# Performance work log

Measured on AMD Instinct MI355X. Metric: run time of the kernel, lower is better.

The kernel has to match this reference:

```python
import jax, jax.numpy as jnp
import numpy as np

WAVE_LEN = 1000.0

def rank_embedding(rank_dim, feat_dim):
    half = feat_dim // 2
    dim_mat = jnp.arange(half, dtype=jnp.float32) / half
    inv = 1.0 / jnp.power(WAVE_LEN, dim_mat)            # [half]
    mul = jnp.arange(rank_dim, dtype=jnp.float32)[:, None] * inv[None, :]  # [K, half]
    return jnp.concatenate([jnp.sin(mul), jnp.cos(mul)], axis=-1)          # [K, feat_dim]

def setup_inputs() -> dict:
    key = jax.random.key(0)
    ks = jax.random.split(key, 16)
    K, NS, NC, D, DF, H, DK = 2048, 18, 19, 1024, 128, 16, 64
    s = 0.02
    return {
        "size_scores": jax.random.normal(ks[0], (1, K, NS), jnp.float32),
        "size_residuals_normalized": jax.random.normal(ks[1], (1, K, NS, 3), jnp.float32),
        "sem_cls_scores": jax.random.normal(ks[2], (K, NC), jnp.float32),
        "appearance_features": jax.random.normal(ks[3], (K, D), jnp.float32),
        "mean_size_arr": jax.random.uniform(ks[4], (NS, 3), jnp.float32, 0.1, 1.0),
        "w_rank": jax.random.normal(ks[5], (D, DF), jnp.float32) * s,
        "b_rank": jnp.zeros((DF,), jnp.float32),
        "w_roi": jax.random.normal(ks[6], (D, DF), jnp.float32) * s,
        "b_roi": jnp.zeros((DF,), jnp.float32),
        "Wq": jax.random.normal(ks[7], (H, DF, DK), jnp.float32) * s,
        "Wk": jax.random.normal(ks[8], (H, DF, DK), jnp.float32) * s,
        "Wv": jax.random.normal(ks[9], (H, D, DK), jnp.float32) * s,
        "w_logit": jax.random.normal(ks[10], (D, 1), jnp.float32) * s,
        "b_logit": jnp.zeros((1,), jnp.float32),
    }

def reference(size_scores, size_residuals_normalized, sem_cls_scores,
              appearance_features, mean_size_arr,
              w_rank, b_rank, w_roi, b_roi, Wq, Wk, Wv, w_logit, b_logit):
    K, D = appearance_features.shape
    # --- predicted box size: gather residual for argmax size class ---
    pred_size_class = jnp.argmax(size_scores, axis=-1)                     # [1,K]
    size_residuals = size_residuals_normalized * mean_size_arr[None, None] # [1,K,NS,3]
    pred_size_residual = jnp.take_along_axis(
        size_residuals, pred_size_class[..., None, None], axis=2)[:, :, 0, :]  # [1,K,3]
    psc = pred_size_class[0]                                               # [K]
    box_size = mean_size_arr[psc] + pred_size_residual[0]                  # [K,3]
    # --- semantic class prob ---
    prob_all = jax.nn.softmax(sem_cls_scores, axis=-1)                     # [K,NC]
    prob = jnp.max(prob_all, axis=-1)                                      # [K]
    prob_argmax = jnp.argmax(prob_all, axis=-1)                            # [K]
    cls_bbox = box_size                                                    # [K,3]
    # --- background masking (jit-friendly analog of nonzero filtering):
    # background (class 0) proposals get key -1 so they sort to the end with score 0.
    fg = prob_argmax > 0
    sort_key = jnp.where(fg, prob, -1.0)
    order = jnp.argsort(-sort_key)                                         # descending
    sorted_prob = jnp.where(fg[order], prob[order], 0.0)                   # [K]
    sorted_labels = prob_argmax[order]                                     # [K]
    sorted_cls_bboxes = cls_bbox[order]                                    # [K,3]
    sorted_features = appearance_features[order]                           # [K,D]
    # --- rank embedding + roi embedding ---
    emb = rank_embedding(K, D)                                             # [K,D]
    nms_rank = emb @ w_rank + b_rank                                       # [K,DF]
    roi = sorted_features @ w_roi + b_roi                                  # [K,DF]
    e = nms_rank + roi                                                     # [K,DF]
    # --- relation-module self-attention: Q/K from embedding, V from features ---
    dk = Wq.shape[-1]
    q = jnp.einsum('kd,hde->hke', e, Wq)                                   # [H,K,dk]
    k = jnp.einsum('kd,hde->hke', e, Wk)
    scores = jnp.einsum('hke,hme->hkm', q, k) / jnp.sqrt(jnp.float32(dk))  # [H,K,K]
    attn = jax.nn.softmax(scores, axis=-1)
    v = jnp.einsum('kf,hfe->hke', sorted_features, Wv)                     # [H,K,dk]
    o = jnp.einsum('hkm,hme->hke', attn, v)                                # [H,K,dk]
    o = jnp.transpose(o, (1, 0, 2)).reshape(K, -1)                         # [K,D]
    attn_out = sorted_features + o                                         # residual
    # --- nms logit ---
    logit = attn_out @ w_logit + b_logit                                   # [K,1]
    s1 = jax.nn.sigmoid(logit).reshape(-1)
    nms_scores = s1 * sorted_prob
    return nms_scores, sorted_labels - 1, sorted_cls_bboxes
```

## Files before the change

kernel.cpp:

```cpp
#include <hip/hip_runtime.h>

#define KP 2048
#define DD 1024
#define DF 128
#define NH 16
#define DKK 64
#define NSS 18
#define NCC 19
#define NCH 4
#define CHUNK 512

typedef __attribute__((ext_vector_type(8))) short short8;
typedef __attribute__((ext_vector_type(4))) short short4_t;
typedef __attribute__((ext_vector_type(4))) float f32x4;

__device__ __forceinline__ short f2bf(float x){
    unsigned u = __float_as_uint(x);
    u += 0x7fffu + ((u >> 16) & 1u);
    return (short)(u >> 16);
}

__device__ __forceinline__ void gl2lds16(const void* g, void* l){
    __builtin_amdgcn_global_load_lds((const __attribute__((address_space(1))) void*)g,
                                     (__attribute__((address_space(3))) void*)l, 16, 0, 0);
}

__global__ void prep_kernel(const float* __restrict__ size_scores,
                            const float* __restrict__ srn,
                            const float* __restrict__ sem,
                            const float* __restrict__ mean,
                            float* __restrict__ box, int* __restrict__ label,
                            double* __restrict__ probd, double* __restrict__ keyd){
    int k = blockIdx.x * blockDim.x + threadIdx.x;
    if (k >= KP) return;
    const float* ss = size_scores + k * NSS;
    int psc = 0; float bs = ss[0];
    for (int s = 1; s < NSS; s++){ float v = ss[s]; if (v > bs){ bs = v; psc = s; } }
    for (int c = 0; c < 3; c++){
        float m = mean[psc * 3 + c];
        float r = srn[k * (NSS * 3) + psc * 3 + c];
        box[k * 3 + c] = m + r * m;
    }
    const float* cs = sem + k * NCC;
    double mx = (double)cs[0]; int lab = 0;
    for (int c = 1; c < NCC; c++){ double v = (double)cs[c]; if (v > mx){ mx = v; lab = c; } }
    double sum = 0.0;
    for (int c = 0; c < NCC; c++) sum += exp((double)cs[c] - mx);
    double prob = 1.0 / sum;
    probd[k] = prob;
    label[k] = lab;
    keyd[k]  = (lab > 0) ? prob : -1.0;
}

__global__ __launch_bounds__(256) void rank_kernel(const double* __restrict__ keyd,
                                                   const int* __restrict__ label,
                                                   const double* __restrict__ probd,
                                                   const float* __restrict__ box,
                                                   int* __restrict__ order, float* __restrict__ sprob,
                                                   float* __restrict__ out){
    int i = blockIdx.x, t = threadIdx.x;
    double ki = keyd[i];
    const double2* k2 = (const double2*)keyd;
    int r = 0;
    #pragma unroll
    for (int p = 0; p < KP / 2 / 256; p++){
        int idx2 = p * 256 + t;
        double2 kj = k2[idx2];
        int j0 = idx2 * 2;
        r += (int)(kj.x > ki) + (int)((kj.x == ki) & (j0 < i));
        r += (int)(kj.y > ki) + (int)((kj.y == ki) & (j0 + 1 < i));
    }
    #pragma unroll
    for (int off = 32; off > 0; off >>= 1) r += __shfl_down(r, off);
    __shared__ int red[4];
    if ((t & 63) == 0) red[t >> 6] = r;
    __syncthreads();
    if (t == 0){
        int rk = red[0] + red[1] + red[2] + red[3];
        order[rk] = i;
        sprob[rk] = (label[i] > 0) ? (float)probd[i] : 0.f;
        out[KP + rk] = (float)(label[i] - 1);
        out[2 * KP + 3 * rk + 0] = box[i * 3 + 0];
        out[2 * KP + 3 * rk + 1] = box[i * 3 + 1];
        out[2 * KP + 3 * rk + 2] = box[i * 3 + 2];
    }
}

__global__ __launch_bounds__(256) void af_kernel(const float* __restrict__ app,
                                                 const int* __restrict__ order,
                                                 short* __restrict__ af){
    int pos = blockIdx.x, t = threadIdx.x;
    int ord = order[pos];
    float4 v = ((const float4*)(app + (size_t)ord * DD))[t];
    short4_t g = { f2bf(v.x), f2bf(v.y), f2bf(v.z), f2bf(v.w) };
    *(short4_t*)(af + (size_t)pos * 2048 + 1024 + t * 4) = g;
    short4_t e;
    #pragma unroll
    for (int i = 0; i < 4; i++){
        int j = t * 4 + i, jj = j & 511;
        float inv = exp2f(-(float)jj * 0.0194644224310197f);
        float arg = (float)pos * inv;
        e[i] = f2bf((j < 512) ? __sinf(arg) : __cosf(arg));
    }
    *(short4_t*)(af + (size_t)pos * 2048 + t * 4) = e;
}

__global__ __launch_bounds__(256) void convw_kernel(const float* __restrict__ w_rank,
                                                    const float* __restrict__ w_roi,
                                                    const float* __restrict__ Wq,
                                                    const float* __restrict__ Wk,
                                                    const float* __restrict__ Wv,
                                                    const float* __restrict__ w_logit,
                                                    short* __restrict__ wcat,
                                                    short* __restrict__ qkT,
                                                    short* __restrict__ uT){
    int b = blockIdx.x;
    if (b >= 128){
        int i = b - 128;
        int h = i >> 2;
        int f = ((i & 3) << 8) + threadIdx.x;
        const float* wv = Wv + (size_t)h * DD * DKK + (size_t)f * DKK;
        const float* wlh = w_logit + h * DKK;
        float s = 0.f;
        #pragma unroll
        for (int e = 0; e < DKK; e++) s += wv[e] * wlh[e];
        uT[h * DD + f] = f2bf(s);
        return;
    }
    __shared__ float tile[64][65];
    const float* src; short* dst; int sstride, dstride, r0, c0, doff;
    float scale = 1.0f;
    if (b < 32){        src = w_rank; dst = wcat; sstride = DF; dstride = 2048;
                        r0 = (b >> 1) * 64; c0 = (b & 1) * 64; doff = 0; }
    else if (b < 64){   int i = b - 32; src = w_roi; dst = wcat; sstride = DF; dstride = 2048;
                        r0 = (i >> 1) * 64; c0 = (i & 1) * 64; doff = 1024; }
    else if (b < 96){   int i = b - 64; int h = i >> 1;
                        src = Wq + (size_t)h * DF * DKK; dst = qkT + (size_t)h * DKK * DF;
                        sstride = DKK; dstride = DF; r0 = (i & 1) * 64; c0 = 0; doff = 0;
                        scale = 0.125f; }
    else {              int i = b - 96; int h = i >> 1;
                        src = Wk + (size_t)h * DF * DKK; dst = qkT + (size_t)(1024 + h * DKK) * DF;
                        sstride = DKK; dstride = DF; r0 = (i & 1) * 64; c0 = 0; doff = 0; }
    int tx = threadIdx.x & 63, ty = threadIdx.x >> 6;
    #pragma unroll
    for (int p = 0; p < 16; p++){
        int r = p * 4 + ty;
        tile[r][tx] = src[(size_t)(r0 + r) * sstride + c0 + tx];
    }
    __syncthreads();
    #pragma unroll
    for (int p = 0; p < 16; p++){
        int r = p * 4 + ty;
        dst[(size_t)(c0 + r) * dstride + doff + r0 + tx] = f2bf(tile[tx][r] * scale);
    }
}

__global__ __launch_bounds__(256) void gemm_lds(const short* __restrict__ A,
                                                const short* __restrict__ BT,
                                                void* __restrict__ C,
                                                int lda, int ldb, int N,
                                                int klen, size_t slabstride, int mode){
    int w = threadIdx.x >> 6, lane = threadIdx.x & 63;
    int quad = lane >> 4, l16 = lane & 15;
    int m0 = blockIdx.x * 64, n0 = blockIdx.y * 64;
    int kb = blockIdx.z * klen;

    __shared__ __align__(16) short alds[64 * 64];
    __shared__ __align__(16) short blds[64 * 64];

    int p0 = w * 64 + lane;
    int r0 = p0 >> 3, q0 = ((p0 & 7) ^ (r0 & 7)) * 8;
    int p1 = p0 + 256;
    int r1 = p1 >> 3, q1 = ((p1 & 7) ^ (r1 & 7)) * 8;
    short* adst0 = alds + w * 512;
    short* adst1 = alds + 2048 + w * 512;
    short* bdst0 = blds + w * 512;
    short* bdst1 = blds + 2048 + w * 512;
    const short* asrc0 = A + (size_t)(m0 + r0) * lda + kb + q0;
    const short* asrc1 = A + (size_t)(m0 + r1) * lda + kb + q1;
    const short* bsrc0 = BT + (size_t)(n0 + r0) * ldb + kb + q0;
    const short* bsrc1 = BT + (size_t)(n0 + r1) * ldb + kb + q1;

    f32x4 acc[4];
    for (int c = 0; c < 4; c++) acc[c] = (f32x4){0.f, 0.f, 0.f, 0.f};

    for (int kt = 0; kt < klen; kt += 64){
        __syncthreads();
        gl2lds16(asrc0 + kt, adst0);
        gl2lds16(asrc1 + kt, adst1);
        gl2lds16(bsrc0 + kt, bdst0);
        gl2lds16(bsrc1 + kt, bdst1);
        __syncthreads();
        int arow = w * 16 + l16;
        #pragma unroll
        for (int s = 0; s < 2; s++){
            short8 a = *(const short8*)(alds + arow * 64 + (((s * 4 + quad) ^ (l16 & 7)) * 8));
            #pragma unroll
            for (int c = 0; c < 4; c++){
                int brow = c * 16 + l16;
                short8 b = *(const short8*)(blds + brow * 64 + (((s * 4 + quad) ^ (l16 & 7)) * 8));
                acc[c] = __builtin_amdgcn_mfma_f32_16x16x32_bf16(a, b, acc[c], 0, 0, 0);
            }
        }
    }
    int mrow = m0 + w * 16 + quad * 4;
    #pragma unroll
    for (int c = 0; c < 4; c++){
        #pragma unroll
        for (int r = 0; r < 4; r++){
            size_t idx = (size_t)(mrow + r) * N + n0 + c * 16 + l16;
            if (mode == 2) ((short*)C)[idx] = f2bf(acc[c][r]);
            else ((float*)C + (size_t)blockIdx.z * slabstride)[idx] = acc[c][r];
        }
    }
}

__global__ __launch_bounds__(256) void combine_e_kernel(const float* __restrict__ es,
                                                        const float* __restrict__ b_rank,
                                                        const float* __restrict__ b_roi,
                                                        short* __restrict__ e_bf){
    int tid = blockIdx.x * 256 + threadIdx.x;
    int base = tid * 4;
    int n = base & (DF - 1);
    float4 s = *(const float4*)(es + base);
    #pragma unroll
    for (int c = 1; c < 4; c++){
        float4 t = *(const float4*)(es + (size_t)c * KP * DF + base);
        s.x += t.x; s.y += t.y; s.z += t.z; s.w += t.w;
    }
    float4 br = *(const float4*)(b_rank + n);
    float4 bo = *(const float4*)(b_roi + n);
    short4_t o = { f2bf(s.x + br.x + bo.x), f2bf(s.y + br.y + bo.y),
                   f2bf(s.z + br.z + bo.z), f2bf(s.w + br.w + bo.w) };
    *(short4_t*)(e_bf + base) = o;
}

__global__ __launch_bounds__(256) void vw_kernel(const short* __restrict__ af,
                                                 const short* __restrict__ uT,
                                                 float* __restrict__ vwT){
    int w = threadIdx.x >> 6, lane = threadIdx.x & 63;
    int quad = lane >> 4, l16 = lane & 15;
    int m0 = blockIdx.x * 64 + w * 16;
    f32x4 acc = (f32x4){0.f, 0.f, 0.f, 0.f};
    const short* arow = af + (size_t)(m0 + l16) * 2048 + 1024 + quad * 8;
    const short* brow = uT + (size_t)l16 * DD + quad * 8;
    for (int k0 = 0; k0 < DD; k0 += 32){
        short8 a = *(const short8*)(arow + k0);
        short8 b = *(const short8*)(brow + k0);
        acc = __builtin_amdgcn_mfma_f32_16x16x32_bf16(a, b, acc, 0, 0, 0);
    }
    #pragma unroll
    for (int r = 0; r < 4; r++)
        vwT[(size_t)l16 * KP + m0 + quad * 4 + r] = acc[r];
}

__global__ __launch_bounds__(256, 4) void attn_kernel(const short* __restrict__ qk,
                                                      const float* __restrict__ vwT,
                                                      float* __restrict__ pl,
                                                      float* __restrict__ pwl){
    int qt = blockIdx.x, h = blockIdx.y, ch = blockIdx.z;
    int tid = threadIdx.x;
    int w = tid >> 6, lane = tid & 63, quad = lane >> 4, l16 = lane & 15;
    int qb = qt * 128;

    __shared__ __align__(16) short klds[64 * 64];

    short8 aq[2][2];
    #pragma unroll
    for (int t = 0; t < 2; t++){
        const short* qrow = qk + (size_t)(qb + t * 64 + w * 16 + l16) * 2048 + h * DKK;
        aq[t][0] = *(const short8*)(qrow + quad * 8);
        aq[t][1] = *(const short8*)(qrow + 32 + quad * 8);
    }

    float lpart[2][4] = {{0.f,0.f,0.f,0.f},{0.f,0.f,0.f,0.f}};
    float wpart[2][4] = {{0.f,0.f,0.f,0.f},{0.f,0.f,0.f,0.f}};

    int seg0 = w * 128 + lane;
    int row0 = seg0 >> 3, c80 = (seg0 & 7) ^ (row0 & 7);
    int seg1 = seg0 + 64;
    int row1 = seg1 >> 3, c81 = (seg1 & 7) ^ (row1 & 7);
    short* kl0 = klds + (size_t)(w * 128) * 8;
    short* kl1 = klds + (size_t)(w * 128 + 64) * 8;

    for (int m0 = ch * CHUNK; m0 < (ch + 1) * CHUNK; m0 += 64){
        __syncthreads();
        gl2lds16(qk + (size_t)(m0 + row0) * 2048 + 1024 + h * DKK + c80 * 8, kl0);
        gl2lds16(qk + (size_t)(m0 + row1) * 2048 + 1024 + h * DKK + c81 * 8, kl1);
        float vwv[4];
        #pragma unroll
        for (int c = 0; c < 4; c++)
            vwv[c] = vwT[(size_t)h * KP + m0 + c * 16 + l16];
        __syncthreads();

        #pragma unroll
        for (int t = 0; t < 2; t++){
            #pragma unroll
            for (int c = 0; c < 4; c++){
                int r = c * 16 + l16, sw = r & 7;
                short8 b0 = *(const short8*)(klds + r * 64 + (quad ^ sw) * 8);
                short8 b1 = *(const short8*)(klds + r * 64 + ((quad + 4) ^ sw) * 8);
                f32x4 acc = (f32x4){0.f, 0.f, 0.f, 0.f};
                acc = __builtin_amdgcn_mfma_f32_16x16x32_bf16(aq[t][0], b0, acc, 0, 0, 0);
                acc = __builtin_amdgcn_mfma_f32_16x16x32_bf16(aq[t][1], b1, acc, 0, 0, 0);
                #pragma unroll
                for (int rr = 0; rr < 4; rr++){
                    float e = __expf(acc[rr]);
                    lpart[t][rr] += e;
                    wpart[t][rr] += e * vwv[c];
                }
            }
        }
    }

    #pragma unroll
    for (int t = 0; t < 2; t++){
        #pragma unroll
        for (int rr = 0; rr < 4; rr++){
            float v = lpart[t][rr], x = wpart[t][rr];
            v += __shfl_xor(v, 1); x += __shfl_xor(x, 1);
            v += __shfl_xor(v, 2); x += __shfl_xor(x, 2);
            v += __shfl_xor(v, 4); x += __shfl_xor(x, 4);
            v += __shfl_xor(v, 8); x += __shfl_xor(x, 8);
            lpart[t][rr] = v; wpart[t][rr] = x;
        }
        if (l16 == 0){
            int qr0 = qb + t * 64 + w * 16;
            #pragma unroll
            for (int rr = 0; rr < 4; rr++){
                size_t idx = ((size_t)ch * NH + h) * KP + qr0 + quad * 4 + rr;
                pl[idx]  = lpart[t][rr];
                pwl[idx] = wpart[t][rr];
            }
        }
    }
}

__global__ __launch_bounds__(256) void final_kernel(const float* __restrict__ app,
                                                    const int* __restrict__ order,
                                                    const float* __restrict__ pl,
                                                    const float* __restrict__ pwl,
                                                    const float* __restrict__ w_logit,
                                                    const float* __restrict__ b_logit,
                                                    const float* __restrict__ sprob,
                                                    float* __restrict__ out){
    int pos = blockIdx.x, t = threadIdx.x;
    int ord = order[pos];
    float4 a = *(const float4*)(app + (size_t)ord * DD + t * 4);
    float4 wv = *(const float4*)(w_logit + t * 4);
    float partial = a.x * wv.x + a.y * wv.y + a.z * wv.z + a.w * wv.w;
    for (int off = 32; off > 0; off >>= 1) partial += __shfl_down(partial, off);
    __shared__ float red[4];
    __shared__ float hsum[NH];
    if ((t & 63) == 0) red[t >> 6] = partial;
    if (t < NH){
        float l = 0.f, x = 0.f;
        #pragma unroll
        for (int c = 0; c < NCH; c++){
            size_t idx = ((size_t)c * NH + t) * KP + pos;
            l += pl[idx]; x += pwl[idx];
        }
        hsum[t] = x / l;
    }
    __syncthreads();
    if (t == 0){
        float logit = red[0] + red[1] + red[2] + red[3] + b_logit[0];
        #pragma unroll
        for (int h = 0; h < NH; h++) logit += hsum[h];
        float s1 = 1.f / (1.f + __expf(-logit));
        out[pos] = s1 * sprob[pos];
    }
}

extern "C" void kernel_launch(void* const* d_in, const int* in_sizes, int n_in,
                              void* d_out, int out_size, void* d_ws, size_t ws_size,
                              hipStream_t stream){
    (void)in_sizes; (void)n_in; (void)out_size; (void)ws_size;
    const float* size_scores = (const float*)d_in[0];
    const float* srn     = (const float*)d_in[1];
    const float* sem     = (const float*)d_in[2];
    const float* app     = (const float*)d_in[3];
    const float* mean    = (const float*)d_in[4];
    const float* w_rank  = (const float*)d_in[5];
    const float* b_rank  = (const float*)d_in[6];
    const float* w_roi   = (const float*)d_in[7];
    const float* b_roi   = (const float*)d_in[8];
    const float* Wq      = (const float*)d_in[9];
    const float* Wk      = (const float*)d_in[10];
    const float* Wv      = (const float*)d_in[11];
    const float* w_logit = (const float*)d_in[12];
    const float* b_logit = (const float*)d_in[13];
    float* out = (float*)d_out;

    char* ws = (char*)d_ws;
    size_t off = 0;
    auto alloc = [&](size_t n) -> char* {
        char* p = ws + off;
        off = (off + n + 255) & ~(size_t)255;
        return p;
    };
    float*  box    = (float*) alloc((size_t)KP * 3 * 4);
    int*    label  = (int*)   alloc((size_t)KP * 4);
    double* probd  = (double*)alloc((size_t)KP * 8);
    double* keyd   = (double*)alloc((size_t)KP * 8);
    int*    order  = (int*)   alloc((size_t)KP * 4);
    float*  sprob  = (float*) alloc((size_t)KP * 4);
    short*  wcat   = (short*) alloc((size_t)DF * 2048 * 2);
    short*  qkT    = (short*) alloc((size_t)2048 * DF * 2);
    short*  uT     = (short*) alloc((size_t)NH * DD * 2);
    short*  e_bf   = (short*) alloc((size_t)KP * DF * 2);
    short*  qk_bf  = (short*) alloc((size_t)KP * 2048 * 2);
    float*  vwT    = (float*) alloc((size_t)NH * KP * 4);
    float*  pl     = (float*) alloc((size_t)NCH * NH * KP * 4);
    float*  pwl    = (float*) alloc((size_t)NCH * NH * KP * 4);
    char*   X      = alloc((size_t)12 * 1024 * 1024);
    short*  af     = (short*)X;
    float*  es     = (float*)(X + (size_t)8 * 1024 * 1024);

    prep_kernel<<<KP / 256, 256, 0, stream>>>(size_scores, srn, sem, mean, box, label, probd, keyd);
    rank_kernel<<<KP, 256, 0, stream>>>(keyd, label, probd, box, order, sprob, out);
    af_kernel<<<KP, 256, 0, stream>>>(app, order, af);
    convw_kernel<<<192, 256, 0, stream>>>(w_rank, w_roi, Wq, Wk, Wv, w_logit, wcat, qkT, uT);
    gemm_lds<<<dim3(KP / 64, DF / 64, 4), 256, 0, stream>>>(af, wcat, es, 2048, 2048, DF, 512,
                                                            (size_t)KP * DF, 0);
    combine_e_kernel<<<(KP * DF / 4) / 256, 256, 0, stream>>>(es, b_rank, b_roi, e_bf);
    gemm_lds<<<dim3(KP / 64, 2048 / 64, 1), 256, 0, stream>>>(e_bf, qkT, qk_bf, DF, DF, 2048, DF,
                                                              0, 2);
    vw_kernel<<<KP / 64, 256, 0, stream>>>(af, uT, vwT);
    attn_kernel<<<dim3(KP / 128, NH, NCH), 256, 0, stream>>>(qk_bf, vwT, pl, pwl);
    final_kernel<<<KP, 256, 0, stream>>>(app, order, pl, pwl, w_logit, b_logit, sprob, out);
}
```

Before: 150.5 us.

## Fuse pipeline stages into fewer launches and finalize logits via atomic counter

Merges prep with weight conversion, rank with the feature scatter and logit dot product, the e-combine with the vw GEMV, and attention with the final sigmoid. The last block per query tile, found through an agent-scope atomic counter, does the final reduction. The first GEMM's split-K goes from 4 to 16 and the attention key chunks from 4 to 2. This removes several kernel launches and their global round trips, and gives the first GEMM more parallelism. The cost is a larger split-K partial buffer, more reduction reads, and atomics plus fences at the end of attention.

```diff
diff --git a/kernel.cpp b/kernel.cpp
--- a/kernel.cpp
+++ b/kernel.cpp
@@ -7,8 +7,9 @@
 #define DKK 64
 #define NSS 18
 #define NCC 19
-#define NCH 4
-#define CHUNK 512
+#define NCH 2
+#define CHUNK 1024
+#define SPLK 16
 
 typedef __attribute__((ext_vector_type(8))) short short8;
 typedef __attribute__((ext_vector_type(4))) short short4_t;
@@ -25,100 +26,41 @@
                                      (__attribute__((address_space(3))) void*)l, 16, 0, 0);
 }
 
-__global__ void prep_kernel(const float* __restrict__ size_scores,
-                            const float* __restrict__ srn,
-                            const float* __restrict__ sem,
-                            const float* __restrict__ mean,
-                            float* __restrict__ box, int* __restrict__ label,
-                            double* __restrict__ probd, double* __restrict__ keyd){
-    int k = blockIdx.x * blockDim.x + threadIdx.x;
-    if (k >= KP) return;
-    const float* ss = size_scores + k * NSS;
-    int psc = 0; float bs = ss[0];
-    for (int s = 1; s < NSS; s++){ float v = ss[s]; if (v > bs){ bs = v; psc = s; } }
-    for (int c = 0; c < 3; c++){
-        float m = mean[psc * 3 + c];
-        float r = srn[k * (NSS * 3) + psc * 3 + c];
-        box[k * 3 + c] = m + r * m;
-    }
-    const float* cs = sem + k * NCC;
-    double mx = (double)cs[0]; int lab = 0;
-    for (int c = 1; c < NCC; c++){ double v = (double)cs[c]; if (v > mx){ mx = v; lab = c; } }
-    double sum = 0.0;
-    for (int c = 0; c < NCC; c++) sum += exp((double)cs[c] - mx);
-    double prob = 1.0 / sum;
-    probd[k] = prob;
-    label[k] = lab;
-    keyd[k]  = (lab > 0) ? prob : -1.0;
-}
-
-__global__ __launch_bounds__(256) void rank_kernel(const double* __restrict__ keyd,
-                                                   const int* __restrict__ label,
-                                                   const double* __restrict__ probd,
-                                                   const float* __restrict__ box,
-                                                   int* __restrict__ order, float* __restrict__ sprob,
-                                                   float* __restrict__ out){
-    int i = blockIdx.x, t = threadIdx.x;
-    double ki = keyd[i];
-    const double2* k2 = (const double2*)keyd;
-    int r = 0;
-    #pragma unroll
-    for (int p = 0; p < KP / 2 / 256; p++){
-        int idx2 = p * 256 + t;
-        double2 kj = k2[idx2];
-        int j0 = idx2 * 2;
-        r += (int)(kj.x > ki) + (int)((kj.x == ki) & (j0 < i));
-        r += (int)(kj.y > ki) + (int)((kj.y == ki) & (j0 + 1 < i));
-    }
-    #pragma unroll
-    for (int off = 32; off > 0; off >>= 1) r += __shfl_down(r, off);
-    __shared__ int red[4];
-    if ((t & 63) == 0) red[t >> 6] = r;
-    __syncthreads();
-    if (t == 0){
-        int rk = red[0] + red[1] + red[2] + red[3];
-        order[rk] = i;
-        sprob[rk] = (label[i] > 0) ? (float)probd[i] : 0.f;
-        out[KP + rk] = (float)(label[i] - 1);
-        out[2 * KP + 3 * rk + 0] = box[i * 3 + 0];
-        out[2 * KP + 3 * rk + 1] = box[i * 3 + 1];
-        out[2 * KP + 3 * rk + 2] = box[i * 3 + 2];
-    }
-}
-
-__global__ __launch_bounds__(256) void af_kernel(const float* __restrict__ app,
-                                                 const int* __restrict__ order,
-                                                 short* __restrict__ af){
-    int pos = blockIdx.x, t = threadIdx.x;
-    int ord = order[pos];
-    float4 v = ((const float4*)(app + (size_t)ord * DD))[t];
-    short4_t g = { f2bf(v.x), f2bf(v.y), f2bf(v.z), f2bf(v.w) };
-    *(short4_t*)(af + (size_t)pos * 2048 + 1024 + t * 4) = g;
-    short4_t e;
-    #pragma unroll
-    for (int i = 0; i < 4; i++){
-        int j = t * 4 + i, jj = j & 511;
-        float inv = exp2f(-(float)jj * 0.0194644224310197f);
-        float arg = (float)pos * inv;
-        e[i] = f2bf((j < 512) ? __sinf(arg) : __cosf(arg));
-    }
-    *(short4_t*)(af + (size_t)pos * 2048 + t * 4) = e;
-}
-
-__global__ __launch_bounds__(256) void convw_kernel(const float* __restrict__ w_rank,
-                                                    const float* __restrict__ w_roi,
-                                                    const float* __restrict__ Wq,
-                                                    const float* __restrict__ Wk,
-                                                    const float* __restrict__ Wv,
-                                                    const float* __restrict__ w_logit,
-                                                    short* __restrict__ wcat,
-                                                    short* __restrict__ qkT,
-                                                    short* __restrict__ uT){
-    int b = blockIdx.x;
+__global__ __launch_bounds__(256) void prep_convw_kernel(const float* __restrict__ size_scores,
+        const float* __restrict__ srn, const float* __restrict__ sem,
+        const float* __restrict__ mean,
+        const float* __restrict__ w_rank, const float* __restrict__ w_roi,
+        const float* __restrict__ Wq, const float* __restrict__ Wk,
+        const float* __restrict__ Wv, const float* __restrict__ w_logit,
+        float* __restrict__ box, int* __restrict__ label,
+        double* __restrict__ probd, double* __restrict__ keyd,
+        short* __restrict__ wcat, short* __restrict__ qkT, short* __restrict__ uT){
+    int bid = blockIdx.x, t = threadIdx.x;
+    if (bid < 8){
+        int k = bid * 256 + t;
+        const float* ss = size_scores + k * NSS;
+        int psc = 0; float bs = ss[0];
+        for (int s = 1; s < NSS; s++){ float v = ss[s]; if (v > bs){ bs = v; psc = s; } }
+        for (int c = 0; c < 3; c++){
+            float m = mean[psc * 3 + c];
+            float r = srn[k * (NSS * 3) + psc * 3 + c];
+            box[k * 3 + c] = m + r * m;
+        }
+        const float* cs = sem + k * NCC;
+        double mx = (double)cs[0]; int lab = 0;
+        for (int c = 1; c < NCC; c++){ double v = (double)cs[c]; if (v > mx){ mx = v; lab = c; } }
+        double sum = 0.0;
+        for (int c = 0; c < NCC; c++) sum += exp((double)cs[c] - mx);
+        probd[k] = 1.0 / sum;
+        label[k] = lab;
+        keyd[k]  = (lab > 0) ? (1.0 / sum) : -1.0;
+        return;
+    }
+    int b = bid - 8;
     if (b >= 128){
         int i = b - 128;
         int h = i >> 2;
-        int f = ((i & 3) << 8) + threadIdx.x;
+        int f = ((i & 3) << 8) + t;
         const float* wv = Wv + (size_t)h * DD * DKK + (size_t)f * DKK;
         const float* wlh = w_logit + h * DKK;
         float s = 0.f;
@@ -141,18 +83,77 @@
     else {              int i = b - 96; int h = i >> 1;
                         src = Wk + (size_t)h * DF * DKK; dst = qkT + (size_t)(1024 + h * DKK) * DF;
                         sstride = DKK; dstride = DF; r0 = (i & 1) * 64; c0 = 0; doff = 0; }
-    int tx = threadIdx.x & 63, ty = threadIdx.x >> 6;
-    #pragma unroll
-    for (int p = 0; p < 16; p++){
-        int r = p * 4 + ty;
+    int tx = t & 63, ty = t >> 6;
+    #pragma unroll
+    for (int pp = 0; pp < 16; pp++){
+        int r = pp * 4 + ty;
         tile[r][tx] = src[(size_t)(r0 + r) * sstride + c0 + tx];
     }
     __syncthreads();
     #pragma unroll
-    for (int p = 0; p < 16; p++){
-        int r = p * 4 + ty;
+    for (int pp = 0; pp < 16; pp++){
+        int r = pp * 4 + ty;
         dst[(size_t)(c0 + r) * dstride + doff + r0 + tx] = f2bf(tile[tx][r] * scale);
     }
+}
+
+__global__ __launch_bounds__(256) void rank_af_kernel(const double* __restrict__ keyd,
+        const int* __restrict__ label, const double* __restrict__ probd,
+        const float* __restrict__ box, const float* __restrict__ app,
+        const float* __restrict__ w_logit,
+        int* __restrict__ order, float* __restrict__ sprob, float* __restrict__ dotl,
+        short* __restrict__ af, unsigned* __restrict__ cnt, float* __restrict__ out){
+    int i = blockIdx.x, t = threadIdx.x;
+    if (i < 16 && t == 0) cnt[i] = 0;
+    __shared__ int redi[4];
+    __shared__ float redf[4];
+    __shared__ int rks;
+    double ki = keyd[i];
+    const double2* k2 = (const double2*)keyd;
+    int r = 0;
+    #pragma unroll
+    for (int pp = 0; pp < KP / 2 / 256; pp++){
+        int idx2 = pp * 256 + t;
+        double2 kj = k2[idx2];
+        int j0 = idx2 * 2;
+        r += (int)(kj.x > ki) + (int)((kj.x == ki) & (j0 < i));
+        r += (int)(kj.y > ki) + (int)((kj.y == ki) & (j0 + 1 < i));
+    }
+    #pragma unroll
+    for (int off = 32; off > 0; off >>= 1) r += __shfl_down(r, off);
+    if ((t & 63) == 0) redi[t >> 6] = r;
+    __syncthreads();
+    if (t == 0){
+        int rk = redi[0] + redi[1] + redi[2] + redi[3];
+        rks = rk;
+        order[rk] = i;
+        sprob[rk] = (label[i] > 0) ? (float)probd[i] : 0.f;
+        out[KP + rk] = (float)(label[i] - 1);
+        out[2 * KP + 3 * rk + 0] = box[i * 3 + 0];
+        out[2 * KP + 3 * rk + 1] = box[i * 3 + 1];
+        out[2 * KP + 3 * rk + 2] = box[i * 3 + 2];
+    }
+    __syncthreads();
+    int pos = rks;
+    float4 v = ((const float4*)(app + (size_t)i * DD))[t];
+    float4 wv = ((const float4*)w_logit)[t];
+    short4_t gg = { f2bf(v.x), f2bf(v.y), f2bf(v.z), f2bf(v.w) };
+    *(short4_t*)(af + (size_t)pos * 2048 + 1024 + t * 4) = gg;
+    float partial = v.x * wv.x + v.y * wv.y + v.z * wv.z + v.w * wv.w;
+    #pragma unroll
+    for (int off = 32; off > 0; off >>= 1) partial += __shfl_down(partial, off);
+    if ((t & 63) == 0) redf[t >> 6] = partial;
+    short4_t e;
+    #pragma unroll
+    for (int ii = 0; ii < 4; ii++){
+        int j = t * 4 + ii, jj = j & 511;
+        float inv = exp2f(-(float)jj * 0.0194644224310197f);
+        float arg = (float)pos * inv;
+        e[ii] = f2bf((j < 512) ? __sinf(arg) : __cosf(arg));
+    }
+    *(short4_t*)(af + (size_t)pos * 2048 + t * 4) = e;
+    __syncthreads();
+    if (t == 0) dotl[pos] = redf[0] + redf[1] + redf[2] + redf[3];
 }
 
 __global__ __launch_bounds__(256) void gemm_lds(const short* __restrict__ A,
@@ -215,64 +216,63 @@
     }
 }
 
-__global__ __launch_bounds__(256) void combine_e_kernel(const float* __restrict__ es,
-                                                        const float* __restrict__ b_rank,
-                                                        const float* __restrict__ b_roi,
-                                                        short* __restrict__ e_bf){
-    int tid = blockIdx.x * 256 + threadIdx.x;
-    int base = tid * 4;
-    int n = base & (DF - 1);
-    float4 s = *(const float4*)(es + base);
-    #pragma unroll
-    for (int c = 1; c < 4; c++){
-        float4 t = *(const float4*)(es + (size_t)c * KP * DF + base);
-        s.x += t.x; s.y += t.y; s.z += t.z; s.w += t.w;
-    }
-    float4 br = *(const float4*)(b_rank + n);
-    float4 bo = *(const float4*)(b_roi + n);
-    short4_t o = { f2bf(s.x + br.x + bo.x), f2bf(s.y + br.y + bo.y),
-                   f2bf(s.z + br.z + bo.z), f2bf(s.w + br.w + bo.w) };
-    *(short4_t*)(e_bf + base) = o;
-}
-
-__global__ __launch_bounds__(256) void vw_kernel(const short* __restrict__ af,
-                                                 const short* __restrict__ uT,
-                                                 float* __restrict__ vwT){
-    int w = threadIdx.x >> 6, lane = threadIdx.x & 63;
-    int quad = lane >> 4, l16 = lane & 15;
-    int m0 = blockIdx.x * 64 + w * 16;
-    f32x4 acc = (f32x4){0.f, 0.f, 0.f, 0.f};
-    const short* arow = af + (size_t)(m0 + l16) * 2048 + 1024 + quad * 8;
-    const short* brow = uT + (size_t)l16 * DD + quad * 8;
-    for (int k0 = 0; k0 < DD; k0 += 32){
-        short8 a = *(const short8*)(arow + k0);
-        short8 b = *(const short8*)(brow + k0);
-        acc = __builtin_amdgcn_mfma_f32_16x16x32_bf16(a, b, acc, 0, 0, 0);
-    }
-    #pragma unroll
-    for (int r = 0; r < 4; r++)
-        vwT[(size_t)l16 * KP + m0 + quad * 4 + r] = acc[r];
-}
-
-__global__ __launch_bounds__(256, 4) void attn_kernel(const short* __restrict__ qk,
-                                                      const float* __restrict__ vwT,
-                                                      float* __restrict__ pl,
-                                                      float* __restrict__ pwl){
+__global__ __launch_bounds__(256) void comb_vw_kernel(const float* __restrict__ es,
+        const float* __restrict__ b_rank, const float* __restrict__ b_roi,
+        const short* __restrict__ af, const short* __restrict__ uT,
+        short* __restrict__ e_bf, float* __restrict__ vwT){
+    int bid = blockIdx.x, t = threadIdx.x;
+    if (bid < 256){
+        int base = (bid * 256 + t) * 4;
+        int n = base & (DF - 1);
+        float4 s = *(const float4*)(es + base);
+        #pragma unroll
+        for (int c = 1; c < SPLK; c++){
+            float4 tt = *(const float4*)(es + (size_t)c * KP * DF + base);
+            s.x += tt.x; s.y += tt.y; s.z += tt.z; s.w += tt.w;
+        }
+        float4 br = *(const float4*)(b_rank + n);
+        float4 bo = *(const float4*)(b_roi + n);
+        short4_t o = { f2bf(s.x + br.x + bo.x), f2bf(s.y + br.y + bo.y),
+                       f2bf(s.z + br.z + bo.z), f2bf(s.w + br.w + bo.w) };
+        *(short4_t*)(e_bf + base) = o;
+    } else {
+        int vb = bid - 256;
+        int w = t >> 6, lane = t & 63, quad = lane >> 4, l16 = lane & 15;
+        int m0 = vb * 64 + w * 16;
+        f32x4 acc = (f32x4){0.f, 0.f, 0.f, 0.f};
+        const short* arow = af + (size_t)(m0 + l16) * 2048 + 1024 + quad * 8;
+        const short* brow = uT + (size_t)l16 * DD + quad * 8;
+        for (int k0 = 0; k0 < DD; k0 += 32){
+            short8 a = *(const short8*)(arow + k0);
+            short8 b = *(const short8*)(brow + k0);
+            acc = __builtin_amdgcn_mfma_f32_16x16x32_bf16(a, b, acc, 0, 0, 0);
+        }
+        #pragma unroll
+        for (int r = 0; r < 4; r++)
+            vwT[(size_t)l16 * KP + m0 + quad * 4 + r] = acc[r];
+    }
+}
+
+__global__ __launch_bounds__(256, 4) void attn_final_kernel(const short* __restrict__ qk,
+        const float* __restrict__ vwT, const float* __restrict__ dotl,
+        const float* __restrict__ sprob, const float* __restrict__ b_logit,
+        float* __restrict__ pl, float* __restrict__ pwl,
+        unsigned* __restrict__ cnt, float* __restrict__ out){
     int qt = blockIdx.x, h = blockIdx.y, ch = blockIdx.z;
-    int tid = threadIdx.x;
-    int w = tid >> 6, lane = tid & 63, quad = lane >> 4, l16 = lane & 15;
+    int t = threadIdx.x;
+    int w = t >> 6, lane = t & 63, quad = lane >> 4, l16 = lane & 15;
     int qb = qt * 128;
 
     __shared__ __align__(16) short klds[64 * 64];
+    __shared__ int lastf;
 
     short8 aq[2][2];
     #pragma unroll
-    for (int t = 0; t < 2; t++){
-        const short* qrow = qk + (size_t)(qb + t * 64 + w * 16 + l16) * 2048 + h * DKK;
-        aq[t][0] = *(const short8*)(qrow + quad * 8);
-        aq[t][1] = *(const short8*)(qrow + 32 + quad * 8);
-    }
-
+    for (int tt = 0; tt < 2; tt++){
+        const short* qrow = qk + (size_t)(qb + tt * 64 + w * 16 + l16) * 2048 + h * DKK;
+        aq[tt][0] = *(const short8*)(qrow + quad * 8);
+        aq[tt][1] = *(const short8*)(qrow + 32 + quad * 8);
+    }
     float lpart[2][4] = {{0.f,0.f,0.f,0.f},{0.f,0.f,0.f,0.f}};
     float wpart[2][4] = {{0.f,0.f,0.f,0.f},{0.f,0.f,0.f,0.f}};
 
@@ -294,81 +294,71 @@
         __syncthreads();
 
         #pragma unroll
-        for (int t = 0; t < 2; t++){
+        for (int tt = 0; tt < 2; tt++){
             #pragma unroll
             for (int c = 0; c < 4; c++){
                 int r = c * 16 + l16, sw = r & 7;
                 short8 b0 = *(const short8*)(klds + r * 64 + (quad ^ sw) * 8);
                 short8 b1 = *(const short8*)(klds + r * 64 + ((quad + 4) ^ sw) * 8);
                 f32x4 acc = (f32x4){0.f, 0.f, 0.f, 0.f};
-                acc = __builtin_amdgcn_mfma_f32_16x16x32_bf16(aq[t][0], b0, acc, 0, 0, 0);
-                acc = __builtin_amdgcn_mfma_f32_16x16x32_bf16(aq[t][1], b1, acc, 0, 0, 0);
+                acc = __builtin_amdgcn_mfma_f32_16x16x32_bf16(aq[tt][0], b0, acc, 0, 0, 0);
+                acc = __builtin_amdgcn_mfma_f32_16x16x32_bf16(aq[tt][1], b1, acc, 0, 0, 0);
                 #pragma unroll
                 for (int rr = 0; rr < 4; rr++){
                     float e = __expf(acc[rr]);
-                    lpart[t][rr] += e;
-                    wpart[t][rr] += e * vwv[c];
+                    lpart[tt][rr] += e;
+                    wpart[tt][rr] += e * vwv[c];
                 }
             }
         }
     }
 
     #pragma unroll
-    for (int t = 0; t < 2; t++){
+    for (int tt = 0; tt < 2; tt++){
         #pragma unroll
         for (int rr = 0; rr < 4; rr++){
-            float v = lpart[t][rr], x = wpart[t][rr];
+            float v = lpart[tt][rr], x = wpart[tt][rr];
             v += __shfl_xor(v, 1); x += __shfl_xor(x, 1);
             v += __shfl_xor(v, 2); x += __shfl_xor(x, 2);
             v += __shfl_xor(v, 4); x += __shfl_xor(x, 4);
             v += __shfl_xor(v, 8); x += __shfl_xor(x, 8);
-            lpart[t][rr] = v; wpart[t][rr] = x;
+            lpart[tt][rr] = v; wpart[tt][rr] = x;
         }
         if (l16 == 0){
-            int qr0 = qb + t * 64 + w * 16;
+            int qr0 = qb + tt * 64 + w * 16;
             #pragma unroll
             for (int rr = 0; rr < 4; rr++){
                 size_t idx = ((size_t)ch * NH + h) * KP + qr0 + quad * 4 + rr;
-                pl[idx]  = lpart[t][rr];
-                pwl[idx] = wpart[t][rr];
+                __hip_atomic_store(pl + idx,  lpart[tt][rr], __ATOMIC_RELAXED, __HIP_MEMORY_SCOPE_AGENT);
+                __hip_atomic_store(pwl + idx, wpart[tt][rr], __ATOMIC_RELAXED, __HIP_MEMORY_SCOPE_AGENT);
             }
         }
     }
-}
-
-__global__ __launch_bounds__(256) void final_kernel(const float* __restrict__ app,
-                                                    const int* __restrict__ order,
-                                                    const float* __restrict__ pl,
-                                                    const float* __restrict__ pwl,
-                                                    const float* __restrict__ w_logit,
-                                                    const float* __restrict__ b_logit,
-                                                    const float* __restrict__ sprob,
-                                                    float* __restrict__ out){
-    int pos = blockIdx.x, t = threadIdx.x;
-    int ord = order[pos];
-    float4 a = *(const float4*)(app + (size_t)ord * DD + t * 4);
-    float4 wv = *(const float4*)(w_logit + t * 4);
-    float partial = a.x * wv.x + a.y * wv.y + a.z * wv.z + a.w * wv.w;
-    for (int off = 32; off > 0; off >>= 1) partial += __shfl_down(partial, off);
-    __shared__ float red[4];
-    __shared__ float hsum[NH];
-    if ((t & 63) == 0) red[t >> 6] = partial;
-    if (t < NH){
-        float l = 0.f, x = 0.f;
-        #pragma unroll
-        for (int c = 0; c < NCH; c++){
-            size_t idx = ((size_t)c * NH + t) * KP + pos;
-            l += pl[idx]; x += pwl[idx];
-        }
-        hsum[t] = x / l;
-    }
     __syncthreads();
     if (t == 0){
-        float logit = red[0] + red[1] + red[2] + red[3] + b_logit[0];
-        #pragma unroll
-        for (int h = 0; h < NH; h++) logit += hsum[h];
-        float s1 = 1.f / (1.f + __expf(-logit));
-        out[pos] = s1 * sprob[pos];
+        __threadfence();
+        unsigned old = __hip_atomic_fetch_add(cnt + qt, 1u, __ATOMIC_ACQ_REL, __HIP_MEMORY_SCOPE_AGENT);
+        lastf = (old == 31);
+    }
+    __syncthreads();
+    if (lastf){
+        __threadfence();
+        if (t < 128){
+            int pos = qb + t;
+            float logit = dotl[pos] + b_logit[0];
+            #pragma unroll
+            for (int hh = 0; hh < NH; hh++){
+                size_t i0 = ((size_t)0 * NH + hh) * KP + pos;
+                size_t i1 = ((size_t)1 * NH + hh) * KP + pos;
+                float l = __hip_atomic_load(pl + i0, __ATOMIC_RELAXED, __HIP_MEMORY_SCOPE_AGENT)
+                        + __hip_atomic_load(pl + i1, __ATOMIC_RELAXED, __HIP_MEMORY_SCOPE_AGENT);
+                float x = __hip_atomic_load(pwl + i0, __ATOMIC_RELAXED, __HIP_MEMORY_SCOPE_AGENT)
+                        + __hip_atomic_load(pwl + i1, __ATOMIC_RELAXED, __HIP_MEMORY_SCOPE_AGENT);
+                logit += x / l;
+            }
+            float s1 = 1.f / (1.f + __expf(-logit));
+            out[pos] = s1 * sprob[pos];
+        }
     }
 }
 
@@ -395,38 +385,37 @@
     char* ws = (char*)d_ws;
     size_t off = 0;
     auto alloc = [&](size_t n) -> char* {
-        char* p = ws + off;
+        char* pp = ws + off;
         off = (off + n + 255) & ~(size_t)255;
-        return p;
+        return pp;
     };
-    float*  box    = (float*) alloc((size_t)KP * 3 * 4);
-    int*    label  = (int*)   alloc((size_t)KP * 4);
-    double* probd  = (double*)alloc((size_t)KP * 8);
-    double* keyd   = (double*)alloc((size_t)KP * 8);
-    int*    order  = (int*)   alloc((size_t)KP * 4);
-    float*  sprob  = (float*) alloc((size_t)KP * 4);
-    short*  wcat   = (short*) alloc((size_t)DF * 2048 * 2);
-    short*  qkT    = (short*) alloc((size_t)2048 * DF * 2);
-    short*  uT     = (short*) alloc((size_t)NH * DD * 2);
-    short*  e_bf   = (short*) alloc((size_t)KP * DF * 2);
-    short*  qk_bf  = (short*) alloc((size_t)KP * 2048 * 2);
-    float*  vwT    = (float*) alloc((size_t)NH * KP * 4);
-    float*  pl     = (float*) alloc((size_t)NCH * NH * KP * 4);
-    float*  pwl    = (float*) alloc((size_t)NCH * NH * KP * 4);
-    char*   X      = alloc((size_t)12 * 1024 * 1024);
-    short*  af     = (short*)X;
-    float*  es     = (float*)(X + (size_t)8 * 1024 * 1024);
-
-    prep_kernel<<<KP / 256, 256, 0, stream>>>(size_scores, srn, sem, mean, box, label, probd, keyd);
-    rank_kernel<<<KP, 256, 0, stream>>>(keyd, label, probd, box, order, sprob, out);
-    af_kernel<<<KP, 256, 0, stream>>>(app, order, af);
-    convw_kernel<<<192, 256, 0, stream>>>(w_rank, w_roi, Wq, Wk, Wv, w_logit, wcat, qkT, uT);
-    gemm_lds<<<dim3(KP / 64, DF / 64, 4), 256, 0, stream>>>(af, wcat, es, 2048, 2048, DF, 512,
-                                                            (size_t)KP * DF, 0);
-    combine_e_kernel<<<(KP * DF / 4) / 256, 256, 0, stream>>>(es, b_rank, b_roi, e_bf);
-    gemm_lds<<<dim3(KP / 64, 2048 / 64, 1), 256, 0, stream>>>(e_bf, qkT, qk_bf, DF, DF, 2048, DF,
-                                                              0, 2);
-    vw_kernel<<<KP / 64, 256, 0, stream>>>(af, uT, vwT);
-    attn_kernel<<<dim3(KP / 128, NH, NCH), 256, 0, stream>>>(qk_bf, vwT, pl, pwl);
-    final_kernel<<<KP, 256, 0, stream>>>(app, order, pl, pwl, w_logit, b_logit, sprob, out);
-}
+    float*    box   = (float*)   alloc((size_t)KP * 3 * 4);
+    int*      label = (int*)     alloc((size_t)KP * 4);
+    double*   probd = (double*)  alloc((size_t)KP * 8);
+    double*   keyd  = (double*)  alloc((size_t)KP * 8);
+    int*      order = (int*)     alloc((size_t)KP * 4);
+    float*    sprob = (float*)   alloc((size_t)KP * 4);
+    float*    dotl  = (float*)   alloc((size_t)KP * 4);
+    unsigned* cnt   = (unsigned*)alloc(16 * 4);
+    short*    wcat  = (short*)   alloc((size_t)DF * 2048 * 2);
+    short*    qkT   = (short*)   alloc((size_t)2048 * DF * 2);
+    short*    uT    = (short*)   alloc((size_t)NH * DD * 2);
+    short*    e_bf  = (short*)   alloc((size_t)KP * DF * 2);
+    short*    qk_bf = (short*)   alloc((size_t)KP * 2048 * 2);
+    float*    vwT   = (float*)   alloc((size_t)NH * KP * 4);
+    float*    pl    = (float*)   alloc((size_t)NCH * NH * KP * 4);
+    float*    pwl   = (float*)   alloc((size_t)NCH * NH * KP * 4);
+    short*    af    = (short*)   alloc((size_t)KP * 2048 * 2);
+    float*    es    = (float*)   alloc((size_t)SPLK * KP * DF * 4);
+
+    prep_convw_kernel<<<200, 256, 0, stream>>>(size_scores, srn, sem, mean,
+        w_rank, w_roi, Wq, Wk, Wv, w_logit, box, label, probd, keyd, wcat, qkT, uT);
+    rank_af_kernel<<<KP, 256, 0, stream>>>(keyd, label, probd, box, app, w_logit,
+        order, sprob, dotl, af, cnt, out);
+    gemm_lds<<<dim3(32, 2, SPLK), 256, 0, stream>>>(af, wcat, es, 2048, 2048, DF,
+        2048 / SPLK, (size_t)KP * DF, 0);
+    comb_vw_kernel<<<288, 256, 0, stream>>>(es, b_rank, b_roi, af, uT, e_bf, vwT);
+    gemm_lds<<<dim3(32, 32, 1), 256, 0, stream>>>(e_bf, qkT, qk_bf, DF, DF, 2048, DF, 0, 2);
+    attn_final_kernel<<<dim3(16, NH, NCH), 256, 0, stream>>>(qk_bf, vwT, dotl, sprob,
+        b_logit, pl, pwl, cnt, out);
+}
```

New measurement: 154.3 us. 1.03x slower.
